# Kernel tuning notes

Hardware: AMD Instinct MI355X
Metric: run time of the kernel (lower is better)

Reference implementation:

```python
import jax, jax.numpy as jnp
import numpy as np

TRACT_SPECS = [
    dict(name="x_a", src_size=4096, dst_size=1024, connections=64, seed=42),
    dict(name="x_b", src_size=4096, dst_size=512, connections=64, seed=43),
    dict(name="x_c", src_size=2048, dst_size=512, connections=32, seed=44),
]


def _make_mask(dst_size, src_size, n_conn, seed):
    rng = np.random.RandomState(seed)
    mask = np.zeros((dst_size, src_size), dtype=np.float32)
    for dst in range(dst_size):
        idx = rng.choice(src_size, size=min(n_conn, src_size), replace=False)
        mask[dst, idx] = 1.0
    return jnp.asarray(mask)


def _xavier_uniform(key, dst, src):
    # matches nn.init.xavier_uniform_ for a (dst, src) weight
    limit = float(np.sqrt(6.0 / (dst + src)))
    return jax.random.uniform(key, (dst, src), jnp.float32, -limit, limit)


def setup_inputs() -> dict:
    key = jax.random.key(0)
    keys = jax.random.split(key, 6)
    B, S = 8, 1024
    inp = {}
    for i, spec in enumerate(TRACT_SPECS):
        src, dst = spec["src_size"], spec["dst_size"]
        inp[spec["name"]] = jax.random.normal(keys[i], (B, S, src), jnp.float32)
        inp["w_" + spec["name"][-1]] = _xavier_uniform(keys[3 + i], dst, src)
        inp["m_" + spec["name"][-1]] = _make_mask(dst, src, spec["connections"], spec["seed"])
    return inp


def reference(x_a, x_b, x_c, w_a, w_b, w_c, m_a, m_b, m_c):
    # Each tract: F.linear(x, weight * mask) -> x @ (W*M)^T; then concat on last dim.
    out_a = jnp.einsum("bsi,oi->bso", x_a, w_a * m_a)
    out_b = jnp.einsum("bsi,oi->bso", x_b, w_b * m_b)
    out_c = jnp.einsum("bsi,oi->bso", x_c, w_c * m_c)
    return jnp.concatenate([out_a, out_b, out_c], axis=-1)
```

## Files before the change

kernel.cpp:

```cpp
#include <hip/hip_runtime.h>
#include <hip/hip_fp16.h>
#include <stdint.h>


#define BS_TOTAL 8192
#define SRC_A 4096
#define SRC_B 4096
#define SRC_C 2048
#define DST_A 1024
#define DST_B 512
#define DST_C 512
#define K_A 64
#define K_B 64
#define K_C 32
#define OUT_DIM 2048
#define LDS_XB_OFF 4096
#define LDS_XC_OFF 8192
#define LDS_TOT 10240


__global__ __launch_bounds__(256) void compress_kernel(
    const float* __restrict__ w_a, const float* __restrict__ m_a,
    const float* __restrict__ w_b, const float* __restrict__ m_b,
    const float* __restrict__ w_c, const float* __restrict__ m_c,
    unsigned* __restrict__ pa, unsigned* __restrict__ pb,
    unsigned* __restrict__ pc) {
    __shared__ int s_cnt;
    __shared__ int s_idx[64];
    __shared__ float s_w[64];
    __shared__ int s_bankcnt[32];
    __shared__ int s_bankoff[32];
    __shared__ unsigned s_sorted[64];

    const int blk = blockIdx.x;
    const int t = threadIdx.x;

    const float *w, *m;
    unsigned* p;
    int dst, src_n, K, DST, lds_off;
    if (blk < DST_A) {
        w = w_a; m = m_a; p = pa; dst = blk;
        src_n = SRC_A; K = K_A; DST = DST_A; lds_off = 0;
    } else if (blk < DST_A + DST_B) {
        w = w_b; m = m_b; p = pb; dst = blk - DST_A;
        src_n = SRC_B; K = K_B; DST = DST_B; lds_off = LDS_XB_OFF;
    } else {
        w = w_c; m = m_c; p = pc; dst = blk - DST_A - DST_B;
        src_n = SRC_C; K = K_C; DST = DST_C; lds_off = LDS_XC_OFF;
    }

    if (t == 0) s_cnt = 0;
    if (t < 32) s_bankcnt[t] = 0;
    __syncthreads();

    const float* mrow = m + (size_t)dst * src_n;
    const float* wrow = w + (size_t)dst * src_n;
    const int per_thread = src_n >> 8;
    for (int i = 0; i < per_thread; ++i) {
        int e = t + (i << 8);
        float mv = mrow[e];
        if (mv != 0.0f) {
            int pos = atomicAdd(&s_cnt, 1);
            if (pos < 64) {
                s_idx[pos] = e;
                s_w[pos] = wrow[e] * mv;
            }
        }
    }
    __syncthreads();
    int cnt = s_cnt;
    if (cnt > K) cnt = K;

    if (t < cnt) atomicAdd(&s_bankcnt[s_idx[t] & 31], 1);
    __syncthreads();
    if (t == 0) {
        int acc = 0;
        for (int b = 0; b < 32; ++b) {
            s_bankoff[b] = acc;
            acc += s_bankcnt[b];
        }
    }
    __syncthreads();
    if (t < cnt) {
        int idx = s_idx[t];
        int j = atomicAdd(&s_bankoff[idx & 31], 1);
        unsigned hb = (unsigned)__half_as_ushort(__float2half(s_w[t]));
        s_sorted[j] = ((unsigned)(lds_off + idx) << 16) | hb;
    }
    __syncthreads();
    if (t >= cnt && t < K) s_sorted[t] = ((unsigned)lds_off << 16);
    __syncthreads();

    if (t < K) {
        int rot = (K == 64) ? ((dst & 31) << 1) : (dst & 31);
        unsigned v = s_sorted[(t + rot) % K];
        p[(size_t)t * DST + dst] = v;
    }
}

__global__ __launch_bounds__(256) void tract_kernel(
    const float* __restrict__ x_a, const float* __restrict__ x_b,
    const float* __restrict__ x_c,
    const unsigned* __restrict__ pa, const unsigned* __restrict__ pb,
    const unsigned* __restrict__ pc,
    float* __restrict__ out) {
    __shared__ unsigned xs[LDS_TOT];
    const int t = threadIdx.x;
    const size_t r0 = (size_t)blockIdx.x * 2;
    const size_t r1 = r0 + 1;

    const float4* a0 = (const float4*)(x_a + r0 * SRC_A);
    const float4* a1 = (const float4*)(x_a + r1 * SRC_A);
    const float4* b0 = (const float4*)(x_b + r0 * SRC_B);
    const float4* b1 = (const float4*)(x_b + r1 * SRC_B);
    const float4* c0 = (const float4*)(x_c + r0 * SRC_C);
    const float4* c1 = (const float4*)(x_c + r1 * SRC_C);
    uint4* xs4 = (uint4*)xs;

#pragma unroll
    for (int i = 0; i < 10; ++i) {
        int q = t + (i << 8);
        const float4 *s0, *s1;
        int qo;
        if (q < 1024)      { s0 = a0; s1 = a1; qo = q; }
        else if (q < 2048) { s0 = b0; s1 = b1; qo = q - 1024; }
        else               { s0 = c0; s1 = c1; qo = q - 2048; }
        float4 v0 = s0[qo];
        float4 v1 = s1[qo];
        uint4 pk;
        __half2 h;
        h = __floats2half2_rn(v0.x, v1.x); pk.x = *(unsigned*)&h;
        h = __floats2half2_rn(v0.y, v1.y); pk.y = *(unsigned*)&h;
        h = __floats2half2_rn(v0.z, v1.z); pk.z = *(unsigned*)&h;
        h = __floats2half2_rn(v0.w, v1.w); pk.w = *(unsigned*)&h;
        xs4[q] = pk;
    }
    __syncthreads();

    float* o0 = out + r0 * OUT_DIM;
    float* o1 = out + r1 * OUT_DIM;

#pragma unroll
    for (int o = 0; o < 4; ++o) {
        int dst = t + (o << 8);
        float acc0 = 0.0f, acc1 = 0.0f;
#pragma unroll 16
        for (int k = 0; k < K_A; ++k) {
            unsigned u = pa[k * DST_A + dst];
            float w = __half2float(__ushort_as_half((unsigned short)(u & 0xffffu)));
            unsigned xv = xs[u >> 16];
            __half2 h = *(__half2*)&xv;
            acc0 += w * __low2float(h);
            acc1 += w * __high2float(h);
        }
        o0[dst] = acc0;
        o1[dst] = acc1;
    }
#pragma unroll
    for (int o = 0; o < 2; ++o) {
        int dst = t + (o << 8);
        float acc0 = 0.0f, acc1 = 0.0f;
#pragma unroll 16
        for (int k = 0; k < K_B; ++k) {
            unsigned u = pb[k * DST_B + dst];
            float w = __half2float(__ushort_as_half((unsigned short)(u & 0xffffu)));
            unsigned xv = xs[u >> 16];
            __half2 h = *(__half2*)&xv;
            acc0 += w * __low2float(h);
            acc1 += w * __high2float(h);
        }
        o0[DST_A + dst] = acc0;
        o1[DST_A + dst] = acc1;
    }
#pragma unroll
    for (int o = 0; o < 2; ++o) {
        int dst = t + (o << 8);
        float acc0 = 0.0f, acc1 = 0.0f;
#pragma unroll 16
        for (int k = 0; k < K_C; ++k) {
            unsigned u = pc[k * DST_C + dst];
            float w = __half2float(__ushort_as_half((unsigned short)(u & 0xffffu)));
            unsigned xv = xs[u >> 16];
            __half2 h = *(__half2*)&xv;
            acc0 += w * __low2float(h);
            acc1 += w * __high2float(h);
        }
        o0[DST_A + DST_B + dst] = acc0;
        o1[DST_A + DST_B + dst] = acc1;
    }
}

extern "C" void kernel_launch(void* const* d_in, const int* in_sizes, int n_in,
                              void* d_out, int out_size, void* d_ws, size_t ws_size,
                              hipStream_t stream) {
    const float* x_a = (const float*)d_in[0];
    const float* w_a = (const float*)d_in[1];
    const float* m_a = (const float*)d_in[2];
    const float* x_b = (const float*)d_in[3];
    const float* w_b = (const float*)d_in[4];
    const float* m_b = (const float*)d_in[5];
    const float* x_c = (const float*)d_in[6];
    const float* w_c = (const float*)d_in[7];
    const float* m_c = (const float*)d_in[8];
    float* out = (float*)d_out;

    char* ws = (char*)d_ws;
    unsigned* pa = (unsigned*)(ws);
    unsigned* pb = (unsigned*)(ws + 262144);
    unsigned* pc = (unsigned*)(ws + 262144 + 131072);

    compress_kernel<<<DST_A + DST_B + DST_C, 256, 0, stream>>>(
        w_a, m_a, w_b, m_b, w_c, m_c, pa, pb, pc);
    tract_kernel<<<BS_TOTAL / 2, 256, 0, stream>>>(x_a, x_b, x_c, pa, pb, pc, out);
}
```

Before: 446.7 us.

## Process four rows per block with 8-byte LDS entries and vectorized packed weights

Each block of the gather kernel now handles four token rows instead of two. The rows are stored in LDS as 8-byte half quads, so one LDS read feeds four FMAs per connection, and each packed weight/index entry is reused across twice as many rows. The compress kernel interleaves its output in groups of four, so the gather loop can fetch connections as uint4 vector loads. Bank-sort buckets change from 32 to 16 to match the wider LDS entries. Output stores become nontemporal. The cost is 80 KB of dynamic LDS per block, half as many blocks, and a static first-call attribute setup.

```diff
diff --git a/kernel.cpp b/kernel.cpp
--- a/kernel.cpp
+++ b/kernel.cpp
@@ -14,9 +14,13 @@
 #define K_B 64
 #define K_C 32
 #define OUT_DIM 2048
-#define LDS_XB_OFF 4096
-#define LDS_XC_OFF 8192
-#define LDS_TOT 10240
+
+#define PAIR_XB_OFF 4096
+#define PAIR_XC_OFF 8192
+#define PAIR_TOT 10240
+#define LDS_BYTES (PAIR_TOT * 8)
+
+typedef float f32x4 __attribute__((ext_vector_type(4)));
 
 
 __global__ __launch_bounds__(256) void compress_kernel(
@@ -28,8 +32,8 @@
     __shared__ int s_cnt;
     __shared__ int s_idx[64];
     __shared__ float s_w[64];
-    __shared__ int s_bankcnt[32];
-    __shared__ int s_bankoff[32];
+    __shared__ int s_bankcnt[16];
+    __shared__ int s_bankoff[16];
     __shared__ unsigned s_sorted[64];
 
     const int blk = blockIdx.x;
@@ -37,20 +41,20 @@
 
     const float *w, *m;
     unsigned* p;
-    int dst, src_n, K, DST, lds_off;
+    int dst, src_n, K, DST, pair_off;
     if (blk < DST_A) {
         w = w_a; m = m_a; p = pa; dst = blk;
-        src_n = SRC_A; K = K_A; DST = DST_A; lds_off = 0;
+        src_n = SRC_A; K = K_A; DST = DST_A; pair_off = 0;
     } else if (blk < DST_A + DST_B) {
         w = w_b; m = m_b; p = pb; dst = blk - DST_A;
-        src_n = SRC_B; K = K_B; DST = DST_B; lds_off = LDS_XB_OFF;
+        src_n = SRC_B; K = K_B; DST = DST_B; pair_off = PAIR_XB_OFF;
     } else {
         w = w_c; m = m_c; p = pc; dst = blk - DST_A - DST_B;
-        src_n = SRC_C; K = K_C; DST = DST_C; lds_off = LDS_XC_OFF;
+        src_n = SRC_C; K = K_C; DST = DST_C; pair_off = PAIR_XC_OFF;
     }
 
     if (t == 0) s_cnt = 0;
-    if (t < 32) s_bankcnt[t] = 0;
+    if (t < 16) s_bankcnt[t] = 0;
     __syncthreads();
 
     const float* mrow = m + (size_t)dst * src_n;
@@ -71,11 +75,11 @@
     int cnt = s_cnt;
     if (cnt > K) cnt = K;
 
-    if (t < cnt) atomicAdd(&s_bankcnt[s_idx[t] & 31], 1);
+    if (t < cnt) atomicAdd(&s_bankcnt[s_idx[t] & 15], 1);
     __syncthreads();
     if (t == 0) {
         int acc = 0;
-        for (int b = 0; b < 32; ++b) {
+        for (int b = 0; b < 16; ++b) {
             s_bankoff[b] = acc;
             acc += s_bankcnt[b];
         }
@@ -83,111 +87,135 @@
     __syncthreads();
     if (t < cnt) {
         int idx = s_idx[t];
-        int j = atomicAdd(&s_bankoff[idx & 31], 1);
+        int j = atomicAdd(&s_bankoff[idx & 15], 1);
         unsigned hb = (unsigned)__half_as_ushort(__float2half(s_w[t]));
-        s_sorted[j] = ((unsigned)(lds_off + idx) << 16) | hb;
-    }
-    __syncthreads();
-    if (t >= cnt && t < K) s_sorted[t] = ((unsigned)lds_off << 16);
+        s_sorted[j] = ((unsigned)(pair_off + idx) << 16) | hb;
+    }
+    __syncthreads();
+    if (t >= cnt && t < K) s_sorted[t] = ((unsigned)pair_off << 16);
     __syncthreads();
 
     if (t < K) {
-        int rot = (K == 64) ? ((dst & 31) << 1) : (dst & 31);
+        int rot = (K == 64) ? ((dst & 15) << 2) : ((dst & 15) << 1);
         unsigned v = s_sorted[(t + rot) % K];
-        p[(size_t)t * DST + dst] = v;
+        p[(((t >> 2) * DST) + dst) * 4 + (t & 3)] = v;
     }
 }
 
-__global__ __launch_bounds__(256) void tract_kernel(
+__global__ __launch_bounds__(256, 2) void tract_kernel(
     const float* __restrict__ x_a, const float* __restrict__ x_b,
     const float* __restrict__ x_c,
     const unsigned* __restrict__ pa, const unsigned* __restrict__ pb,
     const unsigned* __restrict__ pc,
     float* __restrict__ out) {
-    __shared__ unsigned xs[LDS_TOT];
+    extern __shared__ unsigned xs[];
     const int t = threadIdx.x;
-    const size_t r0 = (size_t)blockIdx.x * 2;
-    const size_t r1 = r0 + 1;
-
-    const float4* a0 = (const float4*)(x_a + r0 * SRC_A);
-    const float4* a1 = (const float4*)(x_a + r1 * SRC_A);
-    const float4* b0 = (const float4*)(x_b + r0 * SRC_B);
-    const float4* b1 = (const float4*)(x_b + r1 * SRC_B);
-    const float4* c0 = (const float4*)(x_c + r0 * SRC_C);
-    const float4* c1 = (const float4*)(x_c + r1 * SRC_C);
+    const size_t r0 = (size_t)blockIdx.x * 4;
+
+    const f32x4* a0 = (const f32x4*)(x_a + (r0 + 0) * SRC_A);
+    const f32x4* a1 = (const f32x4*)(x_a + (r0 + 1) * SRC_A);
+    const f32x4* a2 = (const f32x4*)(x_a + (r0 + 2) * SRC_A);
+    const f32x4* a3 = (const f32x4*)(x_a + (r0 + 3) * SRC_A);
+    const f32x4* b0 = (const f32x4*)(x_b + (r0 + 0) * SRC_B);
+    const f32x4* b1 = (const f32x4*)(x_b + (r0 + 1) * SRC_B);
+    const f32x4* b2 = (const f32x4*)(x_b + (r0 + 2) * SRC_B);
+    const f32x4* b3 = (const f32x4*)(x_b + (r0 + 3) * SRC_B);
+    const f32x4* c0 = (const f32x4*)(x_c + (r0 + 0) * SRC_C);
+    const f32x4* c1 = (const f32x4*)(x_c + (r0 + 1) * SRC_C);
+    const f32x4* c2 = (const f32x4*)(x_c + (r0 + 2) * SRC_C);
+    const f32x4* c3 = (const f32x4*)(x_c + (r0 + 3) * SRC_C);
     uint4* xs4 = (uint4*)xs;
 
 #pragma unroll
     for (int i = 0; i < 10; ++i) {
         int q = t + (i << 8);
-        const float4 *s0, *s1;
+        const f32x4 *s0, *s1, *s2, *s3;
         int qo;
-        if (q < 1024)      { s0 = a0; s1 = a1; qo = q; }
-        else if (q < 2048) { s0 = b0; s1 = b1; qo = q - 1024; }
-        else               { s0 = c0; s1 = c1; qo = q - 2048; }
-        float4 v0 = s0[qo];
-        float4 v1 = s1[qo];
-        uint4 pk;
+        if (q < 1024)      { s0 = a0; s1 = a1; s2 = a2; s3 = a3; qo = q; }
+        else if (q < 2048) { s0 = b0; s1 = b1; s2 = b2; s3 = b3; qo = q - 1024; }
+        else               { s0 = c0; s1 = c1; s2 = c2; s3 = c3; qo = q - 2048; }
+        f32x4 v0 = s0[qo];
+        f32x4 v1 = s1[qo];
+        f32x4 v2 = s2[qo];
+        f32x4 v3 = s3[qo];
+        uint4 w0, w1;
         __half2 h;
-        h = __floats2half2_rn(v0.x, v1.x); pk.x = *(unsigned*)&h;
-        h = __floats2half2_rn(v0.y, v1.y); pk.y = *(unsigned*)&h;
-        h = __floats2half2_rn(v0.z, v1.z); pk.z = *(unsigned*)&h;
-        h = __floats2half2_rn(v0.w, v1.w); pk.w = *(unsigned*)&h;
-        xs4[q] = pk;
-    }
-    __syncthreads();
-
-    float* o0 = out + r0 * OUT_DIM;
-    float* o1 = out + r1 * OUT_DIM;
-
-#pragma unroll
+        h = __floats2half2_rn(v0.x, v1.x); w0.x = *(unsigned*)&h;
+        h = __floats2half2_rn(v2.x, v3.x); w0.y = *(unsigned*)&h;
+        h = __floats2half2_rn(v0.y, v1.y); w0.z = *(unsigned*)&h;
+        h = __floats2half2_rn(v2.y, v3.y); w0.w = *(unsigned*)&h;
+        h = __floats2half2_rn(v0.z, v1.z); w1.x = *(unsigned*)&h;
+        h = __floats2half2_rn(v2.z, v3.z); w1.y = *(unsigned*)&h;
+        h = __floats2half2_rn(v0.w, v1.w); w1.z = *(unsigned*)&h;
+        h = __floats2half2_rn(v2.w, v3.w); w1.w = *(unsigned*)&h;
+        xs4[2 * q]     = w0;
+        xs4[2 * q + 1] = w1;
+    }
+    __syncthreads();
+
+    const uint2* xp = (const uint2*)xs;
+    float* o0 = out + (r0 + 0) * OUT_DIM;
+    float* o1 = out + (r0 + 1) * OUT_DIM;
+    float* o2 = out + (r0 + 2) * OUT_DIM;
+    float* o3 = out + (r0 + 3) * OUT_DIM;
+
+#define PROC(u) {                                                            \
+        uint2 xv = xp[(u) >> 16];                                            \
+        float w = __half2float(__ushort_as_half((unsigned short)((u) & 0xffffu))); \
+        const __half2 hlo = *(const __half2*)&xv.x;                          \
+        const __half2 hhi = *(const __half2*)&xv.y;                          \
+        acc0 = fmaf(w, __low2float(hlo), acc0);                              \
+        acc1 = fmaf(w, __high2float(hlo), acc1);                             \
+        acc2 = fmaf(w, __low2float(hhi), acc2);                              \
+        acc3 = fmaf(w, __high2float(hhi), acc3); }
+
+    const uint4* ta = (const uint4*)pa;
+    const uint4* tb = (const uint4*)pb;
+    const uint4* tc = (const uint4*)pc;
+
+#pragma unroll 1
     for (int o = 0; o < 4; ++o) {
         int dst = t + (o << 8);
-        float acc0 = 0.0f, acc1 = 0.0f;
-#pragma unroll 16
-        for (int k = 0; k < K_A; ++k) {
-            unsigned u = pa[k * DST_A + dst];
-            float w = __half2float(__ushort_as_half((unsigned short)(u & 0xffffu)));
-            unsigned xv = xs[u >> 16];
-            __half2 h = *(__half2*)&xv;
-            acc0 += w * __low2float(h);
-            acc1 += w * __high2float(h);
-        }
-        o0[dst] = acc0;
-        o1[dst] = acc1;
-    }
-#pragma unroll
+        float acc0 = 0.0f, acc1 = 0.0f, acc2 = 0.0f, acc3 = 0.0f;
+#pragma unroll
+        for (int k4 = 0; k4 < (K_A >> 2); ++k4) {
+            uint4 e = ta[k4 * DST_A + dst];
+            PROC(e.x) PROC(e.y) PROC(e.z) PROC(e.w)
+        }
+        __builtin_nontemporal_store(acc0, o0 + dst);
+        __builtin_nontemporal_store(acc1, o1 + dst);
+        __builtin_nontemporal_store(acc2, o2 + dst);
+        __builtin_nontemporal_store(acc3, o3 + dst);
+    }
+#pragma unroll 1
     for (int o = 0; o < 2; ++o) {
         int dst = t + (o << 8);
-        float acc0 = 0.0f, acc1 = 0.0f;
-#pragma unroll 16
-        for (int k = 0; k < K_B; ++k) {
-            unsigned u = pb[k * DST_B + dst];
-            float w = __half2float(__ushort_as_half((unsigned short)(u & 0xffffu)));
-            unsigned xv = xs[u >> 16];
-            __half2 h = *(__half2*)&xv;
-            acc0 += w * __low2float(h);
-            acc1 += w * __high2float(h);
-        }
-        o0[DST_A + dst] = acc0;
-        o1[DST_A + dst] = acc1;
-    }
-#pragma unroll
+        float acc0 = 0.0f, acc1 = 0.0f, acc2 = 0.0f, acc3 = 0.0f;
+#pragma unroll
+        for (int k4 = 0; k4 < (K_B >> 2); ++k4) {
+            uint4 e = tb[k4 * DST_B + dst];
+            PROC(e.x) PROC(e.y) PROC(e.z) PROC(e.w)
+        }
+        __builtin_nontemporal_store(acc0, o0 + DST_A + dst);
+        __builtin_nontemporal_store(acc1, o1 + DST_A + dst);
+        __builtin_nontemporal_store(acc2, o2 + DST_A + dst);
+        __builtin_nontemporal_store(acc3, o3 + DST_A + dst);
+    }
+#pragma unroll 1
     for (int o = 0; o < 2; ++o) {
         int dst = t + (o << 8);
-        float acc0 = 0.0f, acc1 = 0.0f;
-#pragma unroll 16
-        for (int k = 0; k < K_C; ++k) {
-            unsigned u = pc[k * DST_C + dst];
-            float w = __half2float(__ushort_as_half((unsigned short)(u & 0xffffu)));
-            unsigned xv = xs[u >> 16];
-            __half2 h = *(__half2*)&xv;
-            acc0 += w * __low2float(h);
-            acc1 += w * __high2float(h);
-        }
-        o0[DST_A + DST_B + dst] = acc0;
-        o1[DST_A + DST_B + dst] = acc1;
-    }
+        float acc0 = 0.0f, acc1 = 0.0f, acc2 = 0.0f, acc3 = 0.0f;
+#pragma unroll
+        for (int k4 = 0; k4 < (K_C >> 2); ++k4) {
+            uint4 e = tc[k4 * DST_C + dst];
+            PROC(e.x) PROC(e.y) PROC(e.z) PROC(e.w)
+        }
+        __builtin_nontemporal_store(acc0, o0 + DST_A + DST_B + dst);
+        __builtin_nontemporal_store(acc1, o1 + DST_A + DST_B + dst);
+        __builtin_nontemporal_store(acc2, o2 + DST_A + DST_B + dst);
+        __builtin_nontemporal_store(acc3, o3 + DST_A + DST_B + dst);
+    }
+#undef PROC
 }
 
 extern "C" void kernel_launch(void* const* d_in, const int* in_sizes, int n_in,
@@ -209,7 +237,14 @@
     unsigned* pb = (unsigned*)(ws + 262144);
     unsigned* pc = (unsigned*)(ws + 262144 + 131072);
 
+    static bool configured = false;
+    if (!configured) {
+        hipFuncSetAttribute(reinterpret_cast<const void*>(&tract_kernel),
+                            hipFuncAttributeMaxDynamicSharedMemorySize, LDS_BYTES);
+        configured = true;
+    }
+
     compress_kernel<<<DST_A + DST_B + DST_C, 256, 0, stream>>>(
         w_a, m_a, w_b, m_b, w_c, m_c, pa, pb, pc);
-    tract_kernel<<<BS_TOTAL / 2, 256, 0, stream>>>(x_a, x_b, x_c, pa, pb, pc, out);
+    tract_kernel<<<BS_TOTAL / 4, 256, LDS_BYTES, stream>>>(x_a, x_b, x_c, pa, pb, pc, out);
 }
```

Measured after the change: 411.5 us. 7.9% less time.
